# Optimization experiments

Hardware: AMD Instinct MI355X
Metric: run time of the kernel (lower is better)

## Reference

```python
import jax, jax.numpy as jnp
import numpy as np
import math

NUM_HEADS = 8
LN_EPS = 1e-5


def layer_norm(x, g, b):
    mu = x.mean(-1, keepdims=True)
    var = ((x - mu) ** 2).mean(-1, keepdims=True)
    return (x - mu) * jax.lax.rsqrt(var + LN_EPS) * g + b


def typed_linear(x, W, types):
    # x: [E, in], W: [R, in, out], types: [E] int -> [E, out]
    out = jnp.zeros((x.shape[0], W.shape[-1]), x.dtype)
    for r in range(W.shape[0]):  # small fixed relation count
        out = out + jnp.where((types == r)[:, None], x @ W[r], 0.0)
    return out


def setup_inputs() -> dict:
    key = jax.random.key(0)
    ks = jax.random.split(key, 20)
    N, M, E = 50000, 10000, 100000
    in_dim, e_dim, out_dim, td = 128, 32, 128, 32
    R, T = 8, 4
    inp = {
        'src_h': jax.random.normal(ks[0], (N, in_dim), jnp.float32),
        'src_tw': jax.random.normal(ks[1], (N, td), jnp.float32),
        'src_tb': jax.random.normal(ks[2], (N, td), jnp.float32),
        'edge_h': jax.random.normal(ks[3], (E, e_dim), jnp.float32),
        'date': jax.random.uniform(ks[4], (E,), jnp.float32),
        'src_idx': jax.random.randint(ks[5], (E,), 0, N, jnp.int32),
        'dst_idx': jax.random.randint(ks[6], (E,), 0, M, jnp.int32),
        'etype': jax.random.randint(ks[7], (E,), 0, R, jnp.int32),
        'ntype': jax.random.randint(ks[8], (M,), 0, T, jnp.int32),
    }
    def w(k, shape):
        return jax.random.normal(k, shape, jnp.float32) / math.sqrt(shape[-2])
    inp['Wq'] = w(ks[9], (R, in_dim, out_dim))
    inp['Wk'] = w(ks[10], (R, in_dim + e_dim, out_dim))
    inp['Wv'] = w(ks[11], (R, in_dim + e_dim, out_dim))
    inp['Wa'] = w(ks[12], (T, out_dim, out_dim))
    inp['h_bias'] = jnp.zeros((T, out_dim), jnp.float32)
    inp['skip'] = jnp.ones((T,), jnp.float32)
    inp['src_ln_g'] = jnp.ones((in_dim + e_dim,), jnp.float32)
    inp['src_ln_b'] = jnp.zeros((in_dim + e_dim,), jnp.float32)
    inp['dst_ln_g'] = jnp.ones((in_dim,), jnp.float32)
    inp['dst_ln_b'] = jnp.zeros((in_dim,), jnp.float32)
    return inp


def reference(src_h, src_tw, src_tb, edge_h, date, src_idx, dst_idx, etype, ntype,
              Wq, Wk, Wv, Wa, h_bias, skip, src_ln_g, src_ln_b, dst_ln_g, dst_ln_b):
    M = ntype.shape[0]
    out_dim = Wq.shape[-1]
    H = NUM_HEADS
    hs = out_dim // H
    td = src_tw.shape[-1]
    t = date[:, None]  # [E,1]

    # gather src / dst node data per edge (dst nodes are first M src rows)
    h_s, tw_s, tb_s = src_h[src_idx], src_tw[src_idx], src_tb[src_idx]
    h_d, tw_d, tb_d = src_h[dst_idx], src_tw[dst_idx], src_tb[dst_idx]

    # time2vec modulation of the first td channels
    dia_s = jnp.concatenate([jnp.sin(tw_s * t + tb_s) * h_s[:, :td], h_s[:, td:]], -1)
    dia_d = jnp.concatenate([jnp.sin(tw_d * t + tb_d) * h_d[:, :td], h_d[:, td:]], -1)
    dia_s = jnp.concatenate([dia_s, edge_h], -1)  # [E, in_dim+e_dim]

    # pre_norm
    dia_s = layer_norm(dia_s, src_ln_g, src_ln_b)
    dia_d = layer_norm(dia_d, dst_ln_g, dst_ln_b)

    q = typed_linear(dia_d, Wq, etype).reshape(-1, H, hs)
    k = typed_linear(dia_s, Wk, etype).reshape(-1, H, hs)
    v = typed_linear(dia_s, Wv, etype).reshape(-1, H, hs)

    a = (q * k).sum(-1) / math.sqrt(out_dim)  # [E, H]

    # edge_softmax: segment softmax over destination nodes
    amax = jax.lax.stop_gradient(jax.ops.segment_max(a, dst_idx, num_segments=M))
    ex = jnp.exp(a - amax[dst_idx])
    denom = jax.ops.segment_sum(ex, dst_idx, num_segments=M)
    alpha = ex / denom[dst_idx]  # [E, H]

    # weighted scatter-sum aggregation
    m = (v * alpha[..., None]).reshape(-1, out_dim)  # [E, out_dim]
    h = jax.ops.segment_sum(m, dst_idx, num_segments=M)  # [M, out_dim]

    h = h + h_bias[ntype]
    gate = jax.nn.sigmoid(skip[ntype])[:, None]
    h = typed_linear(h, Wa, ntype)  # dropout is identity at eval
    dst_h = src_h[:M]
    return h * gate + dst_h * (1.0 - gate)
```

## Files before the change

kernel.cpp:

```cpp
#include <hip/hip_runtime.h>


typedef __attribute__((ext_vector_type(8))) short short8;
typedef __attribute__((ext_vector_type(4))) float f32x4;

__device__ __forceinline__ unsigned short f2bf(float f){
  union { float f; unsigned u; } x; x.f = f;
  unsigned r = x.u + 0x7FFFu + ((x.u >> 16) & 1u);
  return (unsigned short)(r >> 16);
}
__device__ __forceinline__ float bf2f(unsigned short b){
  union { unsigned u; float f; } x; x.u = ((unsigned)b) << 16;
  return x.f;
}


__global__ void k_zero(int* __restrict__ p, int n){
  int i = blockIdx.x*256 + threadIdx.x;
  if(i < n) p[i] = 0;
}

__global__ __launch_bounds__(256) void k_hist(
    const int* __restrict__ etype, const int* __restrict__ dst_idx,
    const int* __restrict__ ntype,
    int* cnt_e, int* cnt_d, int* cnt_n, int E, int M){
  __shared__ int le[8], ln[4];
  int tid = threadIdx.x;
  if(tid < 8) le[tid] = 0;
  if(tid < 4) ln[tid] = 0;
  __syncthreads();
  int g = blockIdx.x*256 + tid;
  if(g < E){ atomicAdd(&le[etype[g]], 1); atomicAdd(&cnt_d[dst_idx[g]], 1); }
  if(g < M){ atomicAdd(&ln[ntype[g]], 1); }
  __syncthreads();
  if(tid < 8 && le[tid]) atomicAdd(&cnt_e[tid], le[tid]);
  if(tid < 4 && ln[tid]) atomicAdd(&cnt_n[tid], ln[tid]);
}

__global__ __launch_bounds__(1024) void k_scan(const int* __restrict__ cnt_e, int* off_e,
                                               const int* __restrict__ cnt_n, int* off_n,
                                               const int* __restrict__ cnt_d, int* off_d, int M){
  __shared__ int part[1024];
  int tid = threadIdx.x;
  if(tid == 0){
    int s = 0;
    for(int i=0;i<8;i++){ off_e[i]=s; s+=cnt_e[i]; } off_e[8]=s;
    s = 0;
    for(int i=0;i<4;i++){ off_n[i]=s; s+=cnt_n[i]; } off_n[4]=s;
  }
  int per = (M + 1023) >> 10;
  int s = 0;
  for(int j=0;j<per;j++){ int idx = tid*per + j; if(idx < M) s += cnt_d[idx]; }
  part[tid] = s; __syncthreads();
  for(int o=1;o<1024;o<<=1){
    int v = (tid >= o) ? part[tid-o] : 0;
    __syncthreads();
    part[tid] += v;
    __syncthreads();
  }
  int run = (tid == 0) ? 0 : part[tid-1];
  for(int j=0;j<per;j++){
    int idx = tid*per + j;
    if(idx < M){ off_d[idx] = run; run += cnt_d[idx]; }
  }
  if(tid == 1023) off_d[M] = run;
}

__global__ __launch_bounds__(256) void k_scatter(
    const int* __restrict__ etype, const int* __restrict__ dst_idx,
    const int* __restrict__ ntype,
    const int* __restrict__ off_e, int* cur_e,
    const int* __restrict__ off_d, int* cur_d,
    const int* __restrict__ off_n, int* cur_n,
    int* eperm, int* dstlist, int* nperm, int* npos, int E, int M){
  __shared__ int lcnt[8], lbase[8], lnc[4], lnb[4];
  int tid = threadIdx.x;
  if(tid < 8) lcnt[tid] = 0;
  if(tid < 4) lnc[tid] = 0;
  __syncthreads();
  int g = blockIdx.x*256 + tid;
  int r = 0, lrank = 0, t = 0, nrank = 0;
  bool inE = (g < E), inM = (g < M);
  if(inE){ r = etype[g]; lrank = atomicAdd(&lcnt[r], 1); }
  if(inM){ t = ntype[g]; nrank = atomicAdd(&lnc[t], 1); }
  __syncthreads();
  if(tid < 8 && lcnt[tid]) lbase[tid] = atomicAdd(&cur_e[tid], lcnt[tid]);
  if(tid < 4 && lnc[tid])  lnb[tid]   = atomicAdd(&cur_n[tid], lnc[tid]);
  __syncthreads();
  if(inE){
    int p = off_e[r] + lbase[r] + lrank;
    eperm[p] = g;
    int d = dst_idx[g];
    int q = off_d[d] + atomicAdd(&cur_d[d], 1);
    dstlist[q] = p;
  }
  if(inM){
    int np = off_n[t] + lnb[t] + nrank;
    npos[g] = np;
    nperm[np] = g;
  }
}

__global__ void k_convw(const float* __restrict__ Wq, const float* __restrict__ Wk,
                        const float* __restrict__ Wv, const float* __restrict__ Wa,
                        unsigned short* Wq_t, unsigned short* Wk_t,
                        unsigned short* Wv_t, unsigned short* Wa_t){
  int tid = blockIdx.x*256 + threadIdx.x;
  if(tid < 131072){
    int r = tid >> 14, rem = tid & 16383, k = rem >> 7, n = rem & 127;
    int nb=n>>4, m=n&15, c=k>>5, quad=(k>>3)&3, j=k&7;
    Wq_t[r*16384 + ((nb*4 + c)*4 + quad)*128 + m*8 + j] = f2bf(Wq[tid]);
  } else if(tid < 294912){
    int u = tid - 131072;
    int r = u / 20480, rem = u - r*20480, k = rem >> 7, n = rem & 127;
    int nb=n>>4, m=n&15, c=k>>5, quad=(k>>3)&3, j=k&7;
    Wk_t[r*20480 + ((nb*5 + c)*4 + quad)*128 + m*8 + j] = f2bf(Wk[u]);
  } else if(tid < 458752){
    int u = tid - 294912;
    int r = u / 20480, rem = u - r*20480, k = rem >> 7, n = rem & 127;
    int nb=n>>4, m=n&15, c=k>>5, quad=(k>>3)&3, j=k&7;
    Wv_t[r*20480 + ((nb*5 + c)*4 + quad)*128 + m*8 + j] = f2bf(Wv[u]);
  } else if(tid < 524288){
    int u = tid - 458752;
    int r = u >> 14, rem = u & 16383, k = rem >> 7, n = rem & 127;
    int nb=n>>4, m=n&15, c=k>>5, quad=(k>>3)&3, j=k&7;
    Wa_t[r*16384 + ((nb*4 + c)*4 + quad)*128 + m*8 + j] = f2bf(Wa[u]);
  }
}

__global__ __launch_bounds__(256) void k_prep(
  const float* __restrict__ src_h, const float* __restrict__ src_tw, const float* __restrict__ src_tb,
  const float* __restrict__ edge_h, const float* __restrict__ date,
  const int* __restrict__ src_idx, const int* __restrict__ dst_idx, const int* __restrict__ eperm,
  const float* __restrict__ g_s, const float* __restrict__ b_s,
  const float* __restrict__ g_d, const float* __restrict__ b_d,
  unsigned short* __restrict__ dia_s, unsigned short* __restrict__ dia_d, int E)
{
  int p = blockIdx.x*8 + (threadIdx.x >> 5);
  if(p >= E) return;
  int l = threadIdx.x & 31;
  int e = eperm[p];
  float t = date[e];
  int s = src_idx[e], d = dst_idx[e];
  float4 hs = *(const float4*)(src_h + (size_t)s*128 + 4*l);
  float4 hd = *(const float4*)(src_h + (size_t)d*128 + 4*l);
  float xe = edge_h[(size_t)e*32 + l];
  float4 sx = hs, dx = hd;
  if(l < 8){
    float4 w4, c4;
    w4 = *(const float4*)(src_tw + (size_t)s*32 + 4*l);
    c4 = *(const float4*)(src_tb + (size_t)s*32 + 4*l);
    sx.x = __sinf(w4.x*t + c4.x) * hs.x;
    sx.y = __sinf(w4.y*t + c4.y) * hs.y;
    sx.z = __sinf(w4.z*t + c4.z) * hs.z;
    sx.w = __sinf(w4.w*t + c4.w) * hs.w;
    w4 = *(const float4*)(src_tw + (size_t)d*32 + 4*l);
    c4 = *(const float4*)(src_tb + (size_t)d*32 + 4*l);
    dx.x = __sinf(w4.x*t + c4.x) * hd.x;
    dx.y = __sinf(w4.y*t + c4.y) * hd.y;
    dx.z = __sinf(w4.z*t + c4.z) * hd.z;
    dx.w = __sinf(w4.w*t + c4.w) * hd.w;
  }
  float s1 = sx.x + sx.y + sx.z + sx.w + xe;
  float s2 = sx.x*sx.x + sx.y*sx.y + sx.z*sx.z + sx.w*sx.w + xe*xe;
  float t1 = dx.x + dx.y + dx.z + dx.w;
  float t2 = dx.x*dx.x + dx.y*dx.y + dx.z*dx.z + dx.w*dx.w;
  #pragma unroll
  for(int i=1;i<32;i<<=1){
    s1 += __shfl_xor(s1,i); s2 += __shfl_xor(s2,i);
    t1 += __shfl_xor(t1,i); t2 += __shfl_xor(t2,i);
  }
  float smu = s1*(1.f/160.f);
  float ssc = rsqrtf(s2*(1.f/160.f) - smu*smu + 1e-5f);
  float dmu = t1*(1.f/128.f);
  float dsc = rsqrtf(t2*(1.f/128.f) - dmu*dmu + 1e-5f);
  float4 gs = *(const float4*)(g_s + 4*l), bs = *(const float4*)(b_s + 4*l);
  float4 gd = *(const float4*)(g_d + 4*l), bd = *(const float4*)(b_d + 4*l);
  unsigned r0 = (unsigned)f2bf((sx.x-smu)*ssc*gs.x + bs.x)
              | ((unsigned)f2bf((sx.y-smu)*ssc*gs.y + bs.y) << 16);
  unsigned r1 = (unsigned)f2bf((sx.z-smu)*ssc*gs.z + bs.z)
              | ((unsigned)f2bf((sx.w-smu)*ssc*gs.w + bs.w) << 16);
  uint2 rs; rs.x = r0; rs.y = r1;
  *(uint2*)(dia_s + (size_t)p*160 + 4*l) = rs;
  dia_s[(size_t)p*160 + 128 + l] = f2bf((xe-smu)*ssc*g_s[128+l] + b_s[128+l]);
  unsigned d0 = (unsigned)f2bf((dx.x-dmu)*dsc*gd.x + bd.x)
              | ((unsigned)f2bf((dx.y-dmu)*dsc*gd.y + bd.y) << 16);
  unsigned d1 = (unsigned)f2bf((dx.z-dmu)*dsc*gd.z + bd.z)
              | ((unsigned)f2bf((dx.w-dmu)*dsc*gd.w + bd.w) << 16);
  uint2 rd; rd.x = d0; rd.y = d1;
  *(uint2*)(dia_d + (size_t)p*128 + 4*l) = rd;
}

template<int NC>
__device__ __forceinline__ void gemm64r8(
  const unsigned short* __restrict__ A, int lda,
  const unsigned short* __restrict__ Wf,
  f32x4* acc, int tid)
{
  int lane = tid & 63, w = tid >> 6, m = lane & 15, quad = lane >> 4;
  const unsigned short* p0 = Wf + (size_t)w*NC*512 + lane*8;
  short8 b0[NC];
  #pragma unroll
  for(int c=0;c<NC;c++) b0[c] = *(const short8*)(p0 + c*512);
  #pragma unroll
  for(int i=0;i<4;i++) acc[i] = (f32x4){0.f,0.f,0.f,0.f};
  #pragma unroll
  for(int c=0;c<NC;c++){
    #pragma unroll
    for(int rt=0; rt<4; rt++){
      short8 af = *(const short8*)(A + (rt*16 + m)*lda + c*32 + quad*8);
      acc[rt] = __builtin_amdgcn_mfma_f32_16x16x32_bf16(af, b0[c], acc[rt], 0,0,0);
    }
  }
}

__global__ __launch_bounds__(512) void k_qkv(
  const unsigned short* __restrict__ dia_d, const unsigned short* __restrict__ dia_s,
  const unsigned short* __restrict__ Wq_t, const unsigned short* __restrict__ Wk_t,
  const unsigned short* __restrict__ Wv_t,
  const int* __restrict__ cnt_e, const int* __restrict__ off_e,
  float* __restrict__ abuf, unsigned short* __restrict__ vbuf)
{
  __shared__ unsigned short Ad[64*136];
  __shared__ unsigned short As[64*168];
  int bid = blockIdx.x;
  int r = -1, tl0 = 0, accT = 0;
  #pragma unroll
  for(int i=0;i<8;i++){
    int n = cnt_e[i], tt = (n + 63) >> 6;
    if(r < 0 && bid < accT + tt){ r = i; tl0 = bid - accT; }
    accT += tt;
  }
  if(r < 0) return;
  int row0 = off_e[r] + tl0*64;
  int nv = min(64, cnt_e[r] - tl0*64);
  int tid = threadIdx.x;
  {
    int4 z = make_int4(0,0,0,0);
    #pragma unroll
    for(int it=0; it<2; it++){
      int idx = it*512 + tid, row = idx >> 4, c = idx & 15;
      int4 v = z;
      if(row < nv) v = *(const int4*)(dia_d + (size_t)(row0+row)*128 + c*8);
      *(int4*)(Ad + row*136 + c*8) = v;
    }
    #pragma unroll
    for(int it=0; it<3; it++){
      int idx = it*512 + tid;
      if(idx < 1280){
        int row = idx/20, c = idx%20;
        int4 v = z;
        if(row < nv) v = *(const int4*)(dia_s + (size_t)(row0+row)*160 + c*8);
        *(int4*)(As + row*168 + c*8) = v;
      }
    }
  }
  __syncthreads();
  int lane = tid & 63, w = tid >> 6, m = lane & 15, quad = lane >> 4;
  f32x4 q[4], kk[4], vv[4];
  gemm64r8<4>(Ad, 136, Wq_t + r*16384, q,  tid);
  gemm64r8<5>(As, 168, Wk_t + r*20480, kk, tid);
  const float inv = 0.08838834764831845f;
  #pragma unroll
  for(int rt=0; rt<4; rt++){
    #pragma unroll
    for(int reg=0; reg<4; reg++){
      float s = q[rt][reg] * kk[rt][reg];
      s += __shfl_xor(s,1); s += __shfl_xor(s,2); s += __shfl_xor(s,4); s += __shfl_xor(s,8);
      int row = rt*16 + quad*4 + reg;
      if(m == 0 && row < nv) abuf[(size_t)(row0+row)*8 + w] = s * inv;
    }
  }
  gemm64r8<5>(As, 168, Wv_t + r*20480, vv, tid);
  #pragma unroll
  for(int rt=0; rt<4; rt++)
  #pragma unroll
  for(int reg=0; reg<4; reg++){
    int row = rt*16 + quad*4 + reg;
    if(row < nv)
      vbuf[(size_t)(row0+row)*128 + w*16 + m] = f2bf(vv[rt][reg]);
  }
}

__global__ __launch_bounds__(128) void k_aggr(
  const float* __restrict__ abuf, const unsigned short* __restrict__ vbuf,
  const int* __restrict__ dstlist, const int* __restrict__ off_d,
  const int* __restrict__ npos, const int* __restrict__ ntype,
  const float* __restrict__ h_bias, unsigned short* __restrict__ hpre)
{
  int d = blockIdx.x, tid = threadIdx.x;
  int o0 = off_d[d], cnt = off_d[d+1] - o0;
  __shared__ float den[8];
  if(tid < 8) den[tid] = 0.f;
  __syncthreads();
  for(int idx = tid; idx < cnt*8; idx += 128){
    int i = idx >> 3, h = idx & 7;
    float ex = __expf(abuf[(size_t)dstlist[o0+i]*8 + h]);
    atomicAdd(&den[h], ex);
  }
  __syncthreads();
  int h = tid >> 4;
  float dh = den[h];
  float rd = (dh > 0.f) ? (1.f/dh) : 0.f;
  float acc = 0.f;
  for(int i=0; i<cnt; i++){
    int p = dstlist[o0+i];
    float al = __expf(abuf[(size_t)p*8 + h]) * rd;
    acc += al * bf2f(vbuf[(size_t)p*128 + tid]);
  }
  int t = ntype[d];
  acc += h_bias[t*128 + tid];
  hpre[(size_t)npos[d]*128 + tid] = f2bf(acc);
}

__global__ __launch_bounds__(512) void k_final(
  const unsigned short* __restrict__ hpre, const unsigned short* __restrict__ Wa_t,
  const int* __restrict__ cnt_n, const int* __restrict__ off_n, const int* __restrict__ nperm,
  const float* __restrict__ skip, const float* __restrict__ src_h, float* __restrict__ out)
{
  __shared__ unsigned short Ah[64*136];
  int bid = blockIdx.x;
  int r = -1, tl0 = 0, accT = 0;
  #pragma unroll
  for(int i=0;i<4;i++){
    int n = cnt_n[i], tt = (n + 63) >> 6;
    if(r < 0 && bid < accT + tt){ r = i; tl0 = bid - accT; }
    accT += tt;
  }
  if(r < 0) return;
  int row0 = off_n[r] + tl0*64;
  int nv = min(64, cnt_n[r] - tl0*64);
  float gate = 1.f / (1.f + __expf(-skip[r]));
  int tid = threadIdx.x;
  int4 z = make_int4(0,0,0,0);
  #pragma unroll
  for(int it=0; it<2; it++){
    int idx = it*512 + tid, row = idx >> 4, c = idx & 15;
    int4 v = z;
    if(row < nv) v = *(const int4*)(hpre + (size_t)(row0+row)*128 + c*8);
    *(int4*)(Ah + row*136 + c*8) = v;
  }
  __syncthreads();
  f32x4 acc[4];
  gemm64r8<4>(Ah, 136, Wa_t + r*16384, acc, tid);
  int lane = tid & 63, w = tid >> 6, m = lane & 15, quad = lane >> 4;
  #pragma unroll
  for(int rt=0; rt<4; rt++)
  #pragma unroll
  for(int reg=0; reg<4; reg++){
    int row = rt*16 + quad*4 + reg;
    if(row < nv){
      int dd = nperm[row0+row];
      int col = w*16 + m;
      out[(size_t)dd*128 + col] = acc[rt][reg]*gate + src_h[(size_t)dd*128 + col]*(1.f - gate);
    }
  }
}

extern "C" void kernel_launch(void* const* d_in, const int* in_sizes, int n_in,
                              void* d_out, int out_size, void* d_ws, size_t ws_size,
                              hipStream_t stream)
{
  const float* src_h  = (const float*)d_in[0];
  const float* src_tw = (const float*)d_in[1];
  const float* src_tb = (const float*)d_in[2];
  const float* edge_h = (const float*)d_in[3];
  const float* date   = (const float*)d_in[4];
  const int*   src_idx= (const int*)d_in[5];
  const int*   dst_idx= (const int*)d_in[6];
  const int*   etype  = (const int*)d_in[7];
  const int*   ntype  = (const int*)d_in[8];
  const float* Wq     = (const float*)d_in[9];
  const float* Wk     = (const float*)d_in[10];
  const float* Wv     = (const float*)d_in[11];
  const float* Wa     = (const float*)d_in[12];
  const float* h_bias = (const float*)d_in[13];
  const float* skip   = (const float*)d_in[14];
  const float* g_s    = (const float*)d_in[15];
  const float* b_s    = (const float*)d_in[16];
  const float* g_d    = (const float*)d_in[17];
  const float* b_d    = (const float*)d_in[18];
  float* out = (float*)d_out;

  const int E = in_sizes[4];
  const int M = in_sizes[8];

  char* base = (char*)d_ws;
  size_t off = 0;
  auto alloc = [&](size_t bytes)->char*{
    off = (off + 255) & ~(size_t)255;
    char* p = base + off; off += bytes; return p;
  };
  int* cnt_e = (int*)alloc((size_t)(24 + 2*M)*4);
  int* cur_e = cnt_e + 8;
  int* cnt_n = cur_e + 8;
  int* cur_n = cnt_n + 4;
  int* cnt_d = cur_n + 4;
  int* cur_d = cnt_d + M;
  const int nzero = 24 + 2*M;
  int* off_e = (int*)alloc(9*4);
  int* off_n = (int*)alloc(5*4);
  int* off_d = (int*)alloc((size_t)(M+1)*4);
  int* eperm   = (int*)alloc((size_t)E*4);
  int* dstlist = (int*)alloc((size_t)E*4);
  int* nperm   = (int*)alloc((size_t)M*4);
  int* npos    = (int*)alloc((size_t)M*4);
  unsigned short* Wq_t = (unsigned short*)alloc((size_t)8*128*128*2);
  unsigned short* Wk_t = (unsigned short*)alloc((size_t)8*160*128*2);
  unsigned short* Wv_t = (unsigned short*)alloc((size_t)8*160*128*2);
  unsigned short* Wa_t = (unsigned short*)alloc((size_t)4*128*128*2);
  unsigned short* dia_d = (unsigned short*)alloc((size_t)E*128*2);
  unsigned short* dia_s = (unsigned short*)alloc((size_t)E*160*2);
  unsigned short* vbuf  = (unsigned short*)alloc((size_t)E*128*2);
  unsigned short* hpre  = (unsigned short*)alloc((size_t)M*128*2);
  float* abuf = (float*)alloc((size_t)E*8*4);

  k_zero<<<dim3((nzero+255)/256), dim3(256), 0, stream>>>(cnt_e, nzero);
  k_hist<<<dim3((E+255)/256), dim3(256), 0, stream>>>(etype, dst_idx, ntype, cnt_e, cnt_d, cnt_n, E, M);
  k_scan<<<dim3(1), dim3(1024), 0, stream>>>(cnt_e, off_e, cnt_n, off_n, cnt_d, off_d, M);
  k_scatter<<<dim3((E+255)/256), dim3(256), 0, stream>>>(etype, dst_idx, ntype,
      off_e, cur_e, off_d, cur_d, off_n, cur_n, eperm, dstlist, nperm, npos, E, M);
  k_convw<<<dim3(2048), dim3(256), 0, stream>>>(Wq, Wk, Wv, Wa, Wq_t, Wk_t, Wv_t, Wa_t);
  k_prep<<<dim3((E+7)/8), dim3(256), 0, stream>>>(src_h, src_tw, src_tb, edge_h, date,
      src_idx, dst_idx, eperm, g_s, b_s, g_d, b_d, dia_s, dia_d, E);
  k_qkv<<<dim3(E/64 + 9), dim3(512), 0, stream>>>(dia_d, dia_s, Wq_t, Wk_t, Wv_t,
      cnt_e, off_e, abuf, vbuf);
  k_aggr<<<dim3(M), dim3(128), 0, stream>>>(abuf, vbuf, dstlist, off_d, npos, ntype, h_bias, hpre);
  k_final<<<dim3(M/64 + 5), dim3(512), 0, stream>>>(hpre, Wa_t, cnt_n, off_n, nperm, skip, src_h, out);
}
```

Measured before the change: 264.6 us.

## Write activations in MFMA fragment layout and drop LDS staging in QKV

The prep kernel now writes dia_s/dia_d directly in the 16-row MFMA fragment-blocked layout, with each edge-type segment padded to a multiple of 64 rows via the offset scan. The QKV kernel then loads A and B fragments straight from global memory with a 2x2 wave tiling, removing the shared-memory staging and its barrier. This trades LDS traffic for more global loads of weight fragments per wave. Padding slots use a zeroed eperm, so padded rows hold edge-0 data and extra prep work is done. The aggregation kernel must still find real edges correctly once offsets include padding.

```diff
diff --git a/kernel.cpp b/kernel.cpp
--- a/kernel.cpp
+++ b/kernel.cpp
@@ -44,7 +44,7 @@
   int tid = threadIdx.x;
   if(tid == 0){
     int s = 0;
-    for(int i=0;i<8;i++){ off_e[i]=s; s+=cnt_e[i]; } off_e[8]=s;
+    for(int i=0;i<8;i++){ off_e[i]=s; s += ((cnt_e[i]+63)>>6)<<6; } off_e[8]=s;
     s = 0;
     for(int i=0;i<4;i++){ off_n[i]=s; s+=cnt_n[i]; } off_n[4]=s;
   }
@@ -134,10 +134,10 @@
   const int* __restrict__ src_idx, const int* __restrict__ dst_idx, const int* __restrict__ eperm,
   const float* __restrict__ g_s, const float* __restrict__ b_s,
   const float* __restrict__ g_d, const float* __restrict__ b_d,
-  unsigned short* __restrict__ dia_s, unsigned short* __restrict__ dia_d, int E)
+  unsigned short* __restrict__ dia_s, unsigned short* __restrict__ dia_d, int Ep)
 {
   int p = blockIdx.x*8 + (threadIdx.x >> 5);
-  if(p >= E) return;
+  if(p >= Ep) return;
   int l = threadIdx.x & 31;
   int e = eperm[p];
   float t = date[e];
@@ -180,37 +180,43 @@
               | ((unsigned)f2bf((sx.y-smu)*ssc*gs.y + bs.y) << 16);
   unsigned r1 = (unsigned)f2bf((sx.z-smu)*ssc*gs.z + bs.z)
               | ((unsigned)f2bf((sx.w-smu)*ssc*gs.w + bs.w) << 16);
-  uint2 rs; rs.x = r0; rs.y = r1;
-  *(uint2*)(dia_s + (size_t)p*160 + 4*l) = rs;
-  dia_s[(size_t)p*160 + 128 + l] = f2bf((xe-smu)*ssc*g_s[128+l] + b_s[128+l]);
   unsigned d0 = (unsigned)f2bf((dx.x-dmu)*dsc*gd.x + bd.x)
               | ((unsigned)f2bf((dx.y-dmu)*dsc*gd.y + bd.y) << 16);
   unsigned d1 = (unsigned)f2bf((dx.z-dmu)*dsc*gd.z + bd.z)
               | ((unsigned)f2bf((dx.w-dmu)*dsc*gd.w + bd.w) << 16);
+  int m = p & 15;
+  int cq = l >> 1;
+  int j  = (4*l) & 7;
+  size_t bs_off = (size_t)(p>>4)*2560;
+  size_t bd_off = (size_t)(p>>4)*2048;
+  uint2 rs; rs.x = r0; rs.y = r1;
   uint2 rd; rd.x = d0; rd.y = d1;
-  *(uint2*)(dia_d + (size_t)p*128 + 4*l) = rd;
+  *(uint2*)(dia_s + bs_off + cq*128 + m*8 + j) = rs;
+  *(uint2*)(dia_d + bd_off + cq*128 + m*8 + j) = rd;
+  dia_s[bs_off + (16 + (l>>3))*128 + m*8 + (l&7)] = f2bf((xe-smu)*ssc*g_s[128+l] + b_s[128+l]);
 }
 
 template<int NC>
-__device__ __forceinline__ void gemm64r8(
-  const unsigned short* __restrict__ A, int lda,
+__device__ __forceinline__ void gemm_nolds(
+  const unsigned short* __restrict__ dia, int fb0,
   const unsigned short* __restrict__ Wf,
-  f32x4* acc, int tid)
-{
-  int lane = tid & 63, w = tid >> 6, m = lane & 15, quad = lane >> 4;
-  const unsigned short* p0 = Wf + (size_t)w*NC*512 + lane*8;
-  short8 b0[NC];
-  #pragma unroll
-  for(int c=0;c<NC;c++) b0[c] = *(const short8*)(p0 + c*512);
+  int rowgrp, int colgrp, int lane, f32x4* acc)
+{
+  const unsigned short* a0 = dia + (size_t)(fb0 + rowgrp*2    )*NC*512 + lane*8;
+  const unsigned short* a1 = dia + (size_t)(fb0 + rowgrp*2 + 1)*NC*512 + lane*8;
+  const unsigned short* b0 = Wf + (size_t)(2*colgrp)*NC*512 + lane*8;
   #pragma unroll
   for(int i=0;i<4;i++) acc[i] = (f32x4){0.f,0.f,0.f,0.f};
   #pragma unroll
   for(int c=0;c<NC;c++){
-    #pragma unroll
-    for(int rt=0; rt<4; rt++){
-      short8 af = *(const short8*)(A + (rt*16 + m)*lda + c*32 + quad*8);
-      acc[rt] = __builtin_amdgcn_mfma_f32_16x16x32_bf16(af, b0[c], acc[rt], 0,0,0);
-    }
+    short8 bf0 = *(const short8*)(b0 + c*512);
+    short8 bf1 = *(const short8*)(b0 + NC*512 + c*512);
+    short8 af0 = *(const short8*)(a0 + c*512);
+    short8 af1 = *(const short8*)(a1 + c*512);
+    acc[0] = __builtin_amdgcn_mfma_f32_16x16x32_bf16(af0, bf0, acc[0], 0,0,0);
+    acc[1] = __builtin_amdgcn_mfma_f32_16x16x32_bf16(af0, bf1, acc[1], 0,0,0);
+    acc[2] = __builtin_amdgcn_mfma_f32_16x16x32_bf16(af1, bf0, acc[2], 0,0,0);
+    acc[3] = __builtin_amdgcn_mfma_f32_16x16x32_bf16(af1, bf1, acc[3], 0,0,0);
   }
 }
 
@@ -221,8 +227,6 @@
   const int* __restrict__ cnt_e, const int* __restrict__ off_e,
   float* __restrict__ abuf, unsigned short* __restrict__ vbuf)
 {
-  __shared__ unsigned short Ad[64*136];
-  __shared__ unsigned short As[64*168];
   int bid = blockIdx.x;
   int r = -1, tl0 = 0, accT = 0;
   #pragma unroll
@@ -235,50 +239,35 @@
   int row0 = off_e[r] + tl0*64;
   int nv = min(64, cnt_e[r] - tl0*64);
   int tid = threadIdx.x;
-  {
-    int4 z = make_int4(0,0,0,0);
-    #pragma unroll
-    for(int it=0; it<2; it++){
-      int idx = it*512 + tid, row = idx >> 4, c = idx & 15;
-      int4 v = z;
-      if(row < nv) v = *(const int4*)(dia_d + (size_t)(row0+row)*128 + c*8);
-      *(int4*)(Ad + row*136 + c*8) = v;
-    }
-    #pragma unroll
-    for(int it=0; it<3; it++){
-      int idx = it*512 + tid;
-      if(idx < 1280){
-        int row = idx/20, c = idx%20;
-        int4 v = z;
-        if(row < nv) v = *(const int4*)(dia_s + (size_t)(row0+row)*160 + c*8);
-        *(int4*)(As + row*168 + c*8) = v;
-      }
-    }
-  }
-  __syncthreads();
   int lane = tid & 63, w = tid >> 6, m = lane & 15, quad = lane >> 4;
+  int rowgrp = w & 1, colgrp = w >> 1;
+  int fb0 = row0 >> 4;
   f32x4 q[4], kk[4], vv[4];
-  gemm64r8<4>(Ad, 136, Wq_t + r*16384, q,  tid);
-  gemm64r8<5>(As, 168, Wk_t + r*20480, kk, tid);
+  gemm_nolds<4>(dia_d, fb0, Wq_t + r*16384, rowgrp, colgrp, lane, q);
+  gemm_nolds<5>(dia_s, fb0, Wk_t + r*20480, rowgrp, colgrp, lane, kk);
   const float inv = 0.08838834764831845f;
   #pragma unroll
-  for(int rt=0; rt<4; rt++){
+  for(int rt=0; rt<2; rt++)
+  #pragma unroll
+  for(int ct=0; ct<2; ct++){
     #pragma unroll
     for(int reg=0; reg<4; reg++){
-      float s = q[rt][reg] * kk[rt][reg];
+      float s = q[rt*2+ct][reg] * kk[rt*2+ct][reg];
       s += __shfl_xor(s,1); s += __shfl_xor(s,2); s += __shfl_xor(s,4); s += __shfl_xor(s,8);
-      int row = rt*16 + quad*4 + reg;
-      if(m == 0 && row < nv) abuf[(size_t)(row0+row)*8 + w] = s * inv;
+      int row = rowgrp*32 + rt*16 + quad*4 + reg;
+      if(m == 0 && row < nv) abuf[(size_t)(row0+row)*8 + colgrp*2 + ct] = s * inv;
     }
   }
-  gemm64r8<5>(As, 168, Wv_t + r*20480, vv, tid);
-  #pragma unroll
-  for(int rt=0; rt<4; rt++)
+  gemm_nolds<5>(dia_s, fb0, Wv_t + r*20480, rowgrp, colgrp, lane, vv);
+  #pragma unroll
+  for(int rt=0; rt<2; rt++)
+  #pragma unroll
+  for(int ct=0; ct<2; ct++)
   #pragma unroll
   for(int reg=0; reg<4; reg++){
-    int row = rt*16 + quad*4 + reg;
+    int row = rowgrp*32 + rt*16 + quad*4 + reg;
     if(row < nv)
-      vbuf[(size_t)(row0+row)*128 + w*16 + m] = f2bf(vv[rt][reg]);
+      vbuf[(size_t)(row0+row)*128 + colgrp*32 + ct*16 + m] = f2bf(vv[rt*2+ct][reg]);
   }
 }
 
@@ -311,6 +300,29 @@
   int t = ntype[d];
   acc += h_bias[t*128 + tid];
   hpre[(size_t)npos[d]*128 + tid] = f2bf(acc);
+}
+
+template<int NC>
+__device__ __forceinline__ void gemm64r8(
+  const unsigned short* __restrict__ A, int lda,
+  const unsigned short* __restrict__ Wf,
+  f32x4* acc, int tid)
+{
+  int lane = tid & 63, w = tid >> 6, m = lane & 15, quad = lane >> 4;
+  const unsigned short* p0 = Wf + (size_t)w*NC*512 + lane*8;
+  short8 b0[NC];
+  #pragma unroll
+  for(int c=0;c<NC;c++) b0[c] = *(const short8*)(p0 + c*512);
+  #pragma unroll
+  for(int i=0;i<4;i++) acc[i] = (f32x4){0.f,0.f,0.f,0.f};
+  #pragma unroll
+  for(int c=0;c<NC;c++){
+    #pragma unroll
+    for(int rt=0; rt<4; rt++){
+      short8 af = *(const short8*)(A + (rt*16 + m)*lda + c*32 + quad*8);
+      acc[rt] = __builtin_amdgcn_mfma_f32_16x16x32_bf16(af, b0[c], acc[rt], 0,0,0);
+    }
+  }
 }
 
 __global__ __launch_bounds__(512) void k_final(
@@ -384,6 +396,7 @@
 
   const int E = in_sizes[4];
   const int M = in_sizes[8];
+  const int Ep = E + 8*63;
 
   char* base = (char*)d_ws;
   size_t off = 0;
@@ -401,7 +414,7 @@
   int* off_e = (int*)alloc(9*4);
   int* off_n = (int*)alloc(5*4);
   int* off_d = (int*)alloc((size_t)(M+1)*4);
-  int* eperm   = (int*)alloc((size_t)E*4);
+  int* eperm   = (int*)alloc((size_t)Ep*4);
   int* dstlist = (int*)alloc((size_t)E*4);
   int* nperm   = (int*)alloc((size_t)M*4);
   int* npos    = (int*)alloc((size_t)M*4);
@@ -409,20 +422,21 @@
   unsigned short* Wk_t = (unsigned short*)alloc((size_t)8*160*128*2);
   unsigned short* Wv_t = (unsigned short*)alloc((size_t)8*160*128*2);
   unsigned short* Wa_t = (unsigned short*)alloc((size_t)4*128*128*2);
-  unsigned short* dia_d = (unsigned short*)alloc((size_t)E*128*2);
-  unsigned short* dia_s = (unsigned short*)alloc((size_t)E*160*2);
-  unsigned short* vbuf  = (unsigned short*)alloc((size_t)E*128*2);
+  unsigned short* dia_d = (unsigned short*)alloc((size_t)(Ep+16)*128*2);
+  unsigned short* dia_s = (unsigned short*)alloc((size_t)(Ep+16)*160*2);
+  unsigned short* vbuf  = (unsigned short*)alloc((size_t)Ep*128*2);
   unsigned short* hpre  = (unsigned short*)alloc((size_t)M*128*2);
-  float* abuf = (float*)alloc((size_t)E*8*4);
+  float* abuf = (float*)alloc((size_t)Ep*8*4);
 
   k_zero<<<dim3((nzero+255)/256), dim3(256), 0, stream>>>(cnt_e, nzero);
+  k_zero<<<dim3((Ep+255)/256), dim3(256), 0, stream>>>(eperm, Ep);
   k_hist<<<dim3((E+255)/256), dim3(256), 0, stream>>>(etype, dst_idx, ntype, cnt_e, cnt_d, cnt_n, E, M);
   k_scan<<<dim3(1), dim3(1024), 0, stream>>>(cnt_e, off_e, cnt_n, off_n, cnt_d, off_d, M);
   k_scatter<<<dim3((E+255)/256), dim3(256), 0, stream>>>(etype, dst_idx, ntype,
       off_e, cur_e, off_d, cur_d, off_n, cur_n, eperm, dstlist, nperm, npos, E, M);
   k_convw<<<dim3(2048), dim3(256), 0, stream>>>(Wq, Wk, Wv, Wa, Wq_t, Wk_t, Wv_t, Wa_t);
-  k_prep<<<dim3((E+7)/8), dim3(256), 0, stream>>>(src_h, src_tw, src_tb, edge_h, date,
-      src_idx, dst_idx, eperm, g_s, b_s, g_d, b_d, dia_s, dia_d, E);
+  k_prep<<<dim3((Ep+7)/8), dim3(256), 0, stream>>>(src_h, src_tw, src_tb, edge_h, date,
+      src_idx, dst_idx, eperm, g_s, b_s, g_d, b_d, dia_s, dia_d, Ep);
   k_qkv<<<dim3(E/64 + 9), dim3(512), 0, stream>>>(dia_d, dia_s, Wq_t, Wk_t, Wv_t,
       cnt_e, off_e, abuf, vbuf);
   k_aggr<<<dim3(M), dim3(128), 0, stream>>>(abuf, vbuf, dstlist, off_d, npos, ntype, h_bias, hpre);
```

New measurement: 260.0 us. Within noise of the previous version (-1.7%).
